# Performance work log

Hardware: AMD Instinct MI355X
Metric: run time of the kernel (lower is better)

Reference implementation:

```python
import jax, jax.numpy as jnp
import numpy as np

B, C, H, W, K = 8, 256, 128, 128, 19  # batch, image channels, spatial, num keypoints


def _uniform_linear(key, out_dim, in_dim):
    # torch nn.Linear default init: U(-1/sqrt(fan_in), 1/sqrt(fan_in))
    bound = 1.0 / np.sqrt(in_dim)
    kw, kb = jax.random.split(key)
    w = jax.random.uniform(kw, (out_dim, in_dim), jnp.float32, -bound, bound)
    b = jax.random.uniform(kb, (out_dim,), jnp.float32, -bound, bound)
    return w, b


def setup_inputs() -> dict:
    key = jax.random.key(0)
    ks = jax.random.split(key, 8)
    image_features = jax.random.normal(ks[0], (B, C, H, W), jnp.float32)
    # keypoints: (x, y, vis). forward computes int((x / W).clamp(0, W-1)), so
    # coords are drawn in [0, W*W) / [0, H*H) to cover the full heatmap grid.
    kx = jax.random.uniform(ks[1], (B, K), jnp.float32, 0.0, float(W * W))
    ky = jax.random.uniform(ks[2], (B, K), jnp.float32, 0.0, float(H * H))
    vis = jax.random.uniform(ks[3], (B, K), jnp.float32)  # >0 => visible
    keypoint_features = jnp.stack([kx, ky, vis], axis=-1)  # [B,K,3]
    img_fc_w, img_fc_b = _uniform_linear(ks[4], C, C)
    kp_proj_w, kp_proj_b = _uniform_linear(ks[5], K, K)  # 1x1 conv == K->K linear over channels
    kp_fc_w, kp_fc_b = _uniform_linear(ks[6], C, K)
    attn_fc_w, attn_fc_b = _uniform_linear(ks[7], 1, C)
    return {
        "image_features": image_features,
        "keypoint_features": keypoint_features,
        "img_fc_w": img_fc_w, "img_fc_b": img_fc_b,
        "kp_proj_w": kp_proj_w, "kp_proj_b": kp_proj_b,
        "kp_fc_w": kp_fc_w, "kp_fc_b": kp_fc_b,
        "attn_fc_w": attn_fc_w, "attn_fc_b": attn_fc_b,
    }


def keypoints_to_heatmap(keypoints, Hh, Ww):
    # Vectorized version of the original nested Python double-loop scatter.
    bsz, nkp, _ = keypoints.shape
    vis = (keypoints[:, :, 2] > 0).astype(jnp.float32)            # [B,K]
    # clamp to [0, dim-1] then truncate to int (values are >=0 so floor==trunc)
    x = jnp.clip(keypoints[:, :, 0] / Ww, 0.0, Ww - 1).astype(jnp.int32)  # [B,K]
    y = jnp.clip(keypoints[:, :, 1] / Hh, 0.0, Hh - 1).astype(jnp.int32)  # [B,K]
    bi = jnp.arange(bsz)[:, None]
    ki = jnp.arange(nkp)[None, :]
    heatmap = jnp.zeros((bsz, nkp, Hh, Ww), jnp.float32)
    # one write per (b,k) -> indices unique across writes; add of 0 for invisible kp
    return heatmap.at[bi, ki, y, x].add(vis)


def reference(image_features, keypoint_features,
              img_fc_w, img_fc_b, kp_proj_w, kp_proj_b,
              kp_fc_w, kp_fc_b, attn_fc_w, attn_fc_b):
    bsz, nch, Hh, Ww = image_features.shape
    heatmap = keypoints_to_heatmap(keypoint_features, Hh, Ww)  # [B,K,H,W]
    # F.interpolate to the same (H,W) with bilinear/align_corners=False maps
    # output pixel i -> input coord i exactly => identity; no-op.
    # keypoint_proj: 1x1 conv over K channels == per-pixel K->K linear
    kp_feat = jnp.einsum('bkhw,ok->bohw', heatmap, kp_proj_w) + kp_proj_b[None, :, None, None]
    img = image_features.reshape(bsz, nch, Hh * Ww).transpose(0, 2, 1)   # [B,S,C]
    kp = kp_feat.reshape(bsz, K, Hh * Ww).transpose(0, 2, 1)             # [B,S,K]
    img_proj = jnp.einsum('bsc,oc->bso', img, img_fc_w) + img_fc_b       # [B,S,C]
    kp_proj = jnp.einsum('bsk,ok->bso', kp, kp_fc_w) + kp_fc_b           # [B,S,C]
    combined = jnp.tanh(img_proj + kp_proj)
    scores = jax.nn.sigmoid(jnp.einsum('bsc,oc->bso', combined, attn_fc_w) + attn_fc_b)  # [B,S,1]
    attended = img * scores                                              # [B,S,C]
    return attended.transpose(0, 2, 1).reshape(bsz, nch, Hh, Ww)
```

## Files before the change

### kernel.cpp

```cpp
#include <hip/hip_runtime.h>
#include <hip/hip_bf16.h>

#define CCH 256
#define HH 128
#define WW 128
#define SS (HH*WW)
#define NB 8
#define NK 19
#define STILE 32
#define NTIL (NB * (SS / STILE))

typedef __attribute__((ext_vector_type(8))) short short8v;
typedef __attribute__((ext_vector_type(4))) float f32x4;

static __device__ __forceinline__ unsigned short f2bf(float x) {
    __hip_bfloat16 h = __float2bfloat16(x);
    return *reinterpret_cast<unsigned short*>(&h);
}
static __device__ __forceinline__ float bf2f(unsigned short u) {
    union { unsigned int i; float f; } z; z.i = ((unsigned int)u) << 16; return z.f;
}
static __device__ __forceinline__ float tanh_fast(float x) {
    float e = __expf(2.f * x);
    return 1.f - 2.f * __builtin_amdgcn_rcpf(e + 1.f);
}
static __device__ __forceinline__ float sigmoid_fast(float z) {
    return __builtin_amdgcn_rcpf(1.f + __expf(-z));
}

__global__ __launch_bounds__(256) void precompute_kernel(
    const float* __restrict__ kf,
    const float* __restrict__ img_fc_w,
    const float* __restrict__ img_fc_b,
    const float* __restrict__ kp_proj_w,
    const float* __restrict__ kp_proj_b,
    const float* __restrict__ kp_fc_w,
    const float* __restrict__ kp_fc_b,
    float* __restrict__ cb,
    float* __restrict__ delta,
    int* __restrict__ pix,
    unsigned short* __restrict__ Wfrag)
{
    int t = threadIdx.x;
    {
        float acc = img_fc_b[t] + kp_fc_b[t];
        for (int k2 = 0; k2 < NK; ++k2) acc += kp_fc_w[t * NK + k2] * kp_proj_b[k2];
        cb[t] = acc;
        for (int k = 0; k < NK; ++k) {
            float d = 0.f;
            for (int k2 = 0; k2 < NK; ++k2) d += kp_fc_w[t * NK + k2] * kp_proj_w[k2 * NK + k];
            delta[t * NK + k] = d;
        }
    }
    if (t < NB * NK) {
        float kx = kf[t * 3 + 0], ky = kf[t * 3 + 1], vis = kf[t * 3 + 2];
        int p = -1;
        if (vis > 0.f) {
            int xi = (int)fminf(fmaxf(kx * (1.f / (float)WW), 0.f), (float)(WW - 1));
            int yi = (int)fminf(fmaxf(ky * (1.f / (float)HH), 0.f), (float)(HH - 1));
            p = yi * WW + xi;
        }
        pix[t] = p;
    }
    for (int g = t; g < 8 * 16 * 64; g += 256) {
        int lane = g & 63;
        int ot = (g >> 6) & 15;
        int ks = g >> 10;
        int o = ot * 16 + (lane & 15);
        int c0 = ks * 32 + (lane >> 4) * 8;
#pragma unroll
        for (int j = 0; j < 8; ++j)
            Wfrag[g * 8 + j] = f2bf(img_fc_w[o * CCH + c0 + j]);
    }
}

__global__ __launch_bounds__(512, 4) void main_kernel(
    const float* __restrict__ img,
    const unsigned short* __restrict__ Wfrag,
    const float* __restrict__ cb,
    const float* __restrict__ aw,
    const float* __restrict__ attn_b,
    float* __restrict__ out)
{
    __shared__ unsigned short Xl[STILE * 256];
    __shared__ float partial[8][STILE];
    __shared__ float scl[STILE];
    __shared__ float cbl[256];
    __shared__ float awl[256];

    const int t = threadIdx.x;
    const int l = t & 63;
    const int w = t >> 6;

    const int bid = blockIdx.x;
    const int swz = (bid & 7) * (NTIL / 8) + (bid >> 3);
    const int b = swz >> 9;
    const int sb = (swz & 511) * STILE;
    const float* imgb = img + (size_t)b * CCH * SS;

    if (t < 256) { cbl[t] = cb[t]; awl[t] = aw[t]; }

    const int pq = (t & 15) * 2;
    const int cg = t >> 4;
    const int c0 = cg * 8;

    {
        float2 xf2[8];
#pragma unroll
        for (int j = 0; j < 8; ++j)
            xf2[j] = *reinterpret_cast<const float2*>(imgb + (size_t)(c0 + j) * SS + sb + pq);
#pragma unroll
        for (int p = 0; p < 2; ++p) {
            int s = pq + p;
            short8v pk;
#pragma unroll
            for (int j = 0; j < 8; ++j)
                pk[j] = (short)f2bf(p ? xf2[j].y : xf2[j].x);
            int idx = s * 256 + ((cg ^ (s & 7)) << 3);
            *reinterpret_cast<short8v*>(&Xl[idx]) = pk;
        }
    }
    __syncthreads();

    f32x4 acc[2][2];
#pragma unroll
    for (int m = 0; m < 2; ++m)
#pragma unroll
        for (int n = 0; n < 2; ++n)
            acc[m][n] = (f32x4){0.f, 0.f, 0.f, 0.f};

#pragma unroll
    for (int ks = 0; ks < 8; ++ks) {
        short8v a[2], bf[2];
#pragma unroll
        for (int m = 0; m < 2; ++m)
            a[m] = *reinterpret_cast<const short8v*>(
                &Wfrag[(((ks * 16 + (w * 2 + m)) * 64) + l) * 8]);
        const int cblk = ks * 4 + (l >> 4);
#pragma unroll
        for (int n = 0; n < 2; ++n) {
            int s = n * 16 + (l & 15);
            bf[n] = *reinterpret_cast<const short8v*>(
                &Xl[s * 256 + ((cblk ^ (s & 7)) << 3)]);
        }
#pragma unroll
        for (int m = 0; m < 2; ++m)
#pragma unroll
            for (int n = 0; n < 2; ++n)
                acc[m][n] = __builtin_amdgcn_mfma_f32_16x16x32_bf16(a[m], bf[n], acc[m][n], 0, 0, 0);
    }

    float p2[2];
#pragma unroll
    for (int n = 0; n < 2; ++n) {
        float accp = 0.f;
#pragma unroll
        for (int m = 0; m < 2; ++m)
#pragma unroll
            for (int r = 0; r < 4; ++r) {
                int o = (w * 2 + m) * 16 + ((l >> 4) << 2) + r;
                accp += awl[o] * tanh_fast(acc[m][n][r] + cbl[o]);
            }
        accp += __shfl_xor(accp, 16);
        accp += __shfl_xor(accp, 32);
        p2[n] = accp;
    }
    if (l < 16) {
        partial[w][l] = p2[0];
        partial[w][16 + l] = p2[1];
    }
    __syncthreads();
    if (t < STILE) {
        float z = attn_b[0];
#pragma unroll
        for (int ww = 0; ww < 8; ++ww) z += partial[ww][t];
        scl[t] = sigmoid_fast(z);
    }
    __syncthreads();

    {
        float s0 = scl[pq], s1 = scl[pq + 1];
        short8v v0, v1;
        {
            int i0 = pq * 256 + ((cg ^ (pq & 7)) << 3);
            int i1 = (pq + 1) * 256 + ((cg ^ ((pq + 1) & 7)) << 3);
            v0 = *reinterpret_cast<const short8v*>(&Xl[i0]);
            v1 = *reinterpret_cast<const short8v*>(&Xl[i1]);
        }
#pragma unroll
        for (int j = 0; j < 8; ++j) {
            float2 o2;
            o2.x = bf2f((unsigned short)v0[j]) * s0;
            o2.y = bf2f((unsigned short)v1[j]) * s1;
            *reinterpret_cast<float2*>(
                out + (size_t)(b * CCH + c0 + j) * SS + sb + pq) = o2;
        }
    }
}

__global__ __launch_bounds__(256) void fixup_kernel(
    const float* __restrict__ img,
    const float* __restrict__ img_fc_w,
    const float* __restrict__ aw,
    const float* __restrict__ attn_b,
    const float* __restrict__ cb,
    const float* __restrict__ delta,
    const int* __restrict__ pix,
    float* __restrict__ out)
{
    int bk = blockIdx.x;
    int b = bk / NK;
    int p = pix[bk];
    if (p < 0) return;
    __shared__ float x[256];
    __shared__ float red[256];
    __shared__ float ssc;
    int t = threadIdx.x;
    const float* imgb = img + (size_t)b * CCH * SS;
    x[t] = imgb[(size_t)t * SS + p];
    __syncthreads();
    float dsum = 0.f;
    for (int k2 = 0; k2 < NK; ++k2)
        if (pix[b * NK + k2] == p) dsum += delta[t * NK + k2];
    float acc = cb[t] + dsum;
    for (int c = 0; c < CCH; ++c) acc += img_fc_w[t * CCH + c] * x[c];
    red[t] = aw[t] * tanh_fast(acc);
    __syncthreads();
    for (int off = 128; off > 0; off >>= 1) {
        if (t < off) red[t] += red[t + off];
        __syncthreads();
    }
    if (t == 0) ssc = sigmoid_fast(red[0] + attn_b[0]);
    __syncthreads();
    out[(size_t)(b * CCH + t) * SS + p] = x[t] * ssc;
}

extern "C" void kernel_launch(void* const* d_in, const int* in_sizes, int n_in,
                              void* d_out, int out_size, void* d_ws, size_t ws_size,
                              hipStream_t stream) {
    (void)in_sizes; (void)n_in; (void)out_size; (void)ws_size;
    const float* img       = (const float*)d_in[0];
    const float* kf        = (const float*)d_in[1];
    const float* img_fc_w  = (const float*)d_in[2];
    const float* img_fc_b  = (const float*)d_in[3];
    const float* kp_proj_w = (const float*)d_in[4];
    const float* kp_proj_b = (const float*)d_in[5];
    const float* kp_fc_w   = (const float*)d_in[6];
    const float* kp_fc_b   = (const float*)d_in[7];
    const float* attn_fc_w = (const float*)d_in[8];
    const float* attn_fc_b = (const float*)d_in[9];
    float* out = (float*)d_out;

    char* ws = (char*)d_ws;
    float* cb             = (float*)(ws);
    float* delta          = (float*)(ws + 1024);
    int*   pix            = (int*)  (ws + 20480);
    unsigned short* Wfrag = (unsigned short*)(ws + 21504);

    precompute_kernel<<<1, 256, 0, stream>>>(kf, img_fc_w, img_fc_b, kp_proj_w,
                                             kp_proj_b, kp_fc_w, kp_fc_b,
                                             cb, delta, pix, Wfrag);
    main_kernel<<<NTIL, 512, 0, stream>>>(img, Wfrag, cb,
                                          attn_fc_w, attn_fc_b, out);
    fixup_kernel<<<NB * NK, 256, 0, stream>>>(img, img_fc_w, attn_fc_w, attn_fc_b,
                                              cb, delta, pix, out);
}
```

Measured before the change: 83.71 us.

## Stage image tile in LDS via async global-to-LDS loads, output full-precision values

The main kernel now copies the fp32 image tile straight into shared memory with global_load_lds instead of staging it through registers. It then builds the bf16 MFMA operand from that copy, and the final output reads the original fp32 values rather than the bf16 round-trip. The score reduction is done redundantly per thread, which drops one barrier and the scl array, and output stores are marked nontemporal. This should cut register pressure and load latency, but shared memory use grows by 32KB per block, which may reduce occupancy below the 4 blocks requested in launch bounds.

```diff
diff --git a/kernel.cpp b/kernel.cpp
--- a/kernel.cpp
+++ b/kernel.cpp
@@ -17,15 +17,17 @@
     __hip_bfloat16 h = __float2bfloat16(x);
     return *reinterpret_cast<unsigned short*>(&h);
 }
-static __device__ __forceinline__ float bf2f(unsigned short u) {
-    union { unsigned int i; float f; } z; z.i = ((unsigned int)u) << 16; return z.f;
-}
 static __device__ __forceinline__ float tanh_fast(float x) {
     float e = __expf(2.f * x);
     return 1.f - 2.f * __builtin_amdgcn_rcpf(e + 1.f);
 }
 static __device__ __forceinline__ float sigmoid_fast(float z) {
     return __builtin_amdgcn_rcpf(1.f + __expf(-z));
+}
+static __device__ __forceinline__ void gload_lds16(const float* g, float* l) {
+    __builtin_amdgcn_global_load_lds(
+        (const __attribute__((address_space(1))) void*)g,
+        (__attribute__((address_space(3))) void*)l, 16, 0, 0);
 }
 
 __global__ __launch_bounds__(256) void precompute_kernel(
@@ -82,9 +84,9 @@
     const float* __restrict__ attn_b,
     float* __restrict__ out)
 {
+    __shared__ float Xf[CCH * STILE];
     __shared__ unsigned short Xl[STILE * 256];
     __shared__ float partial[8][STILE];
-    __shared__ float scl[STILE];
     __shared__ float cbl[256];
     __shared__ float awl[256];
 
@@ -98,25 +100,29 @@
     const int sb = (swz & 511) * STILE;
     const float* imgb = img + (size_t)b * CCH * SS;
 
+#pragma unroll
+    for (int i = 0; i < 4; ++i) {
+        const int c0 = w * 32 + i * 8;
+        gload_lds16(imgb + (size_t)(c0 + (l >> 3)) * SS + sb + (l & 7) * 4,
+                    &Xf[c0 * STILE]);
+    }
+
     if (t < 256) { cbl[t] = cb[t]; awl[t] = aw[t]; }
-
-    const int pq = (t & 15) * 2;
-    const int cg = t >> 4;
-    const int c0 = cg * 8;
-
+    __syncthreads();
+
+    const int sl = t & 31;
+    const int cg16 = (t >> 5) * 16;
     {
-        float2 xf2[8];
-#pragma unroll
-        for (int j = 0; j < 8; ++j)
-            xf2[j] = *reinterpret_cast<const float2*>(imgb + (size_t)(c0 + j) * SS + sb + pq);
-#pragma unroll
-        for (int p = 0; p < 2; ++p) {
-            int s = pq + p;
+        float xv[16];
+#pragma unroll
+        for (int j = 0; j < 16; ++j) xv[j] = Xf[(cg16 + j) * STILE + sl];
+#pragma unroll
+        for (int h = 0; h < 2; ++h) {
             short8v pk;
 #pragma unroll
-            for (int j = 0; j < 8; ++j)
-                pk[j] = (short)f2bf(p ? xf2[j].y : xf2[j].x);
-            int idx = s * 256 + ((cg ^ (s & 7)) << 3);
+            for (int e = 0; e < 8; ++e) pk[e] = (short)f2bf(xv[h * 8 + e]);
+            int cblk = (cg16 >> 3) + h;
+            int idx = sl * 256 + ((cblk ^ (sl & 7)) << 3);
             *reinterpret_cast<short8v*>(&Xl[idx]) = pk;
         }
     }
@@ -170,30 +176,17 @@
         partial[w][16 + l] = p2[1];
     }
     __syncthreads();
-    if (t < STILE) {
+
+    {
         float z = attn_b[0];
 #pragma unroll
-        for (int ww = 0; ww < 8; ++ww) z += partial[ww][t];
-        scl[t] = sigmoid_fast(z);
-    }
-    __syncthreads();
-
-    {
-        float s0 = scl[pq], s1 = scl[pq + 1];
-        short8v v0, v1;
-        {
-            int i0 = pq * 256 + ((cg ^ (pq & 7)) << 3);
-            int i1 = (pq + 1) * 256 + ((cg ^ ((pq + 1) & 7)) << 3);
-            v0 = *reinterpret_cast<const short8v*>(&Xl[i0]);
-            v1 = *reinterpret_cast<const short8v*>(&Xl[i1]);
-        }
-#pragma unroll
-        for (int j = 0; j < 8; ++j) {
-            float2 o2;
-            o2.x = bf2f((unsigned short)v0[j]) * s0;
-            o2.y = bf2f((unsigned short)v1[j]) * s1;
-            *reinterpret_cast<float2*>(
-                out + (size_t)(b * CCH + c0 + j) * SS + sb + pq) = o2;
+        for (int ww = 0; ww < 8; ++ww) z += partial[ww][sl];
+        const float sc = sigmoid_fast(z);
+#pragma unroll
+        for (int j = 0; j < 16; ++j) {
+            float v = Xf[(cg16 + j) * STILE + sl];
+            __builtin_nontemporal_store(
+                v * sc, out + (size_t)(b * CCH + cg16 + j) * SS + sb + sl);
         }
     }
 }
@@ -232,7 +225,7 @@
     }
     if (t == 0) ssc = sigmoid_fast(red[0] + attn_b[0]);
     __syncthreads();
-    out[(size_t)(b * CCH + t) * SS + p] = x[t] * ssc;
+    __builtin_nontemporal_store(x[t] * ssc, out + (size_t)(b * CCH + t) * SS + p);
 }
 
 extern "C" void kernel_launch(void* const* d_in, const int* in_sizes, int n_in,
```

Result: no change. 83.46 us (-0.3%).
